# Kernel optimization log

Hardware: AMD Instinct MI355X
Metric: run time of the kernel (lower is better)

Reference implementation:

```python
import jax, jax.numpy as jnp
import numpy as np

N = 8192
NHID = 256

def setup_inputs() -> dict:
    key = jax.random.key(0)
    ks = jax.random.split(key, 9)
    s = 1.0 / np.sqrt(NHID)  # torch Linear default init scale
    return {
        "x1": jax.random.normal(ks[0], (N, NHID), jnp.float32),
        "x2": jax.random.normal(ks[1], (N, NHID), jnp.float32),
        "x3": jax.random.normal(ks[2], (N, NHID), jnp.float32),
        "Wq": jax.random.uniform(ks[3], (NHID, NHID), jnp.float32, -s, s),
        "bq": jax.random.uniform(ks[4], (NHID,), jnp.float32, -s, s),
        "Wk": jax.random.uniform(ks[5], (NHID, NHID), jnp.float32, -s, s),
        "bk": jax.random.uniform(ks[6], (NHID,), jnp.float32, -s, s),
        "Wv": jax.random.uniform(ks[7], (NHID, NHID), jnp.float32, -s, s),
        "bv": jax.random.uniform(ks[8], (NHID,), jnp.float32, -s, s),
    }

def reference(x1, x2, x3, Wq, bq, Wk, bk, Wv, bv):
    # torch.nn.Linear: y = x @ W.T + b
    q = x1 @ Wq.T + bq                      # [N, nhid]
    k = x2 @ Wk.T + bk                      # [N, nhid]
    v = x3 @ Wv.T + bv                      # [N, nhid]
    scores = q @ k.T                        # [N, N], NOTE: unscaled (no 1/sqrt(d))
    attn = jax.nn.softmax(scores, axis=1)   # softmax over keys (dim=1)
    return attn @ v                         # [N, nhid]
```

## Files before the change

### kernel.cpp

```cpp
#include <hip/hip_runtime.h>
#include <stdint.h>

typedef unsigned short u16;
typedef __attribute__((ext_vector_type(8))) short short8;
typedef __attribute__((ext_vector_type(4))) float f32x4;

#define LOG2E 1.4426950408889634f
#define NT 8192
#define DH 256

#define QH     0
#define KH     2097152
#define VTB    4194304
#define OPARTB 6291456
#define XH0 6291456
#define XL0 8388608
#define XH1 10485760
#define XL1 12582912
#define XH2 14680064
#define XL2 16777216
#define WQH 18874368
#define WQL 18939904
#define WKH 19005440
#define WKL 19070976
#define WVH 19136512
#define WVL 19202048
#define MPART_F 11534336
#define LPART_F 11599872

__device__ __forceinline__ u16 f2bf(float f) {
  union { float f; uint32_t u; } c; c.f = f;
  uint32_t u = c.u;
  return (u16)((u + 0x7fffu + ((u >> 16) & 1)) >> 16);
}
__device__ __forceinline__ u16 f2bf_hu(float f) {
  union { float f; uint32_t u; } c; c.f = f;
  return (u16)((c.u + 0x8000u) >> 16);
}
__device__ __forceinline__ float bf2f(u16 h) {
  union { uint32_t u; float f; } c; c.u = ((uint32_t)h) << 16;
  return c.f;
}

__device__ __forceinline__ int swz32(int u, int row) {
  return (u & 24) | ((u & 7) ^ (row & 7));
}

__device__ __forceinline__ f32x4 mfma16(short8 a, short8 b, f32x4 c) {
  return __builtin_amdgcn_mfma_f32_16x16x32_bf16(a, b, c, 0, 0, 0);
}

__device__ __forceinline__ void gl_lds16(const u16* g, u16* l) {
  __builtin_amdgcn_global_load_lds(
      (const __attribute__((address_space(1))) uint32_t*)g,
      (__attribute__((address_space(3))) uint32_t*)l, 16, 0, 0);
}

__global__ __launch_bounds__(256) void k_convert(
    const float* __restrict__ x1, const float* __restrict__ x2, const float* __restrict__ x3,
    const float* __restrict__ wq, const float* __restrict__ wk, const float* __restrict__ wv,
    u16* __restrict__ wsu) {
  int b = blockIdx.x;
  const float* src; u16 *dh, *dl; int bl;
  if (b < 1024)      { src = x1; dh = wsu + XH0; dl = wsu + XL0; bl = b; }
  else if (b < 2048) { src = x2; dh = wsu + XH1; dl = wsu + XL1; bl = b - 1024; }
  else if (b < 3072) { src = x3; dh = wsu + XH2; dl = wsu + XL2; bl = b - 2048; }
  else if (b < 3104) { src = wq; dh = wsu + WQH; dl = wsu + WQL; bl = b - 3072; }
  else if (b < 3136) { src = wk; dh = wsu + WKH; dl = wsu + WKL; bl = b - 3104; }
  else               { src = wv; dh = wsu + WVH; dl = wsu + WVL; bl = b - 3136; }
  int i = (bl * 256 + threadIdx.x) * 8;
  f32x4 a = *(const f32x4*)(src + i);
  f32x4 c = *(const f32x4*)(src + i + 4);
  short8 rh, rl;
  float v[8] = {a[0], a[1], a[2], a[3], c[0], c[1], c[2], c[3]};
#pragma unroll
  for (int j = 0; j < 8; j++) {
    u16 h = f2bf(v[j]);
    rh[j] = (short)h;
    rl[j] = (short)f2bf(v[j] - bf2f(h));
  }
  *(short8*)(dh + i) = rh;
  *(short8*)(dl + i) = rl;
}

__global__ __launch_bounds__(256) void k_qkv(
    u16* __restrict__ wsu,
    const float* __restrict__ bq, const float* __restrict__ bk, const float* __restrict__ bv) {
  __shared__ u16 sAh[32 * 256];
  __shared__ u16 sAl[32 * 256];
  int bx = blockIdx.x;
  int mid = bx >> 8;
  int t = bx & 255;
  const u16 *Ah, *Al, *Bh, *Bl; u16 *O; const float* bias;
  int rowA0, col0, ldO, biasRow;
  if (mid == 0) {
    Ah = wsu + XH0; Al = wsu + XL0; Bh = wsu + WQH; Bl = wsu + WQL;
    O = wsu + QH; bias = bq; biasRow = 0; ldO = 256;
    rowA0 = t * 32; col0 = 0;
  } else if (mid == 1) {
    Ah = wsu + XH1; Al = wsu + XL1; Bh = wsu + WKH; Bl = wsu + WKL;
    O = wsu + KH; bias = bk; biasRow = 0; ldO = 256;
    rowA0 = t * 32; col0 = 0;
  } else {
    Ah = wsu + WVH; Al = wsu + WVL; Bh = wsu + XH2; Bl = wsu + XL2;
    O = wsu + VTB; bias = bv; biasRow = 1; ldO = 8192;
    rowA0 = (t & 7) * 32; col0 = (t >> 3) * 256;
  }

  int tid = threadIdx.x;
#pragma unroll
  for (int i = 0; i < 4; i++) {
    int L = i * 256 + tid;
    int row = L >> 5, u = L & 31;
    short8 vh = *(const short8*)(Ah + (size_t)(rowA0 + row) * 256 + u * 8);
    short8 vl = *(const short8*)(Al + (size_t)(rowA0 + row) * 256 + u * 8);
    *(short8*)(&sAh[row * 256 + swz32(u, row) * 8]) = vh;
    *(short8*)(&sAl[row * 256 + swz32(u, row) * 8]) = vl;
  }
  __syncthreads();

  int lane = tid & 63, wave = tid >> 6;
  int n = lane & 15, quad = lane >> 4;

#pragma unroll 1
  for (int itc = 0; itc < 4; itc++) {
    int colg = col0 + itc * 64 + wave * 16 + n;
    const u16* pBh = Bh + (size_t)colg * 256 + quad * 8;
    const u16* pBl = Bl + (size_t)colg * 256 + quad * 8;
    f32x4 acc0 = {0.f,0.f,0.f,0.f}, acc1 = {0.f,0.f,0.f,0.f};
#pragma unroll
    for (int kk = 0; kk < 8; kk++) {
      int su = swz32(kk * 4 + quad, n) * 8;
      short8 a0h = *(const short8*)(&sAh[n * 256 + su]);
      short8 a1h = *(const short8*)(&sAh[(n + 16) * 256 + su]);
      short8 a0l = *(const short8*)(&sAl[n * 256 + su]);
      short8 a1l = *(const short8*)(&sAl[(n + 16) * 256 + su]);
      short8 bh  = *(const short8*)(pBh + kk * 32);
      short8 bl  = *(const short8*)(pBl + kk * 32);
      acc0 = mfma16(a0h, bh, acc0);
      acc1 = mfma16(a1h, bh, acc1);
      acc0 = mfma16(a0h, bl, acc0);
      acc1 = mfma16(a1h, bl, acc1);
      acc0 = mfma16(a0l, bh, acc0);
      acc1 = mfma16(a1l, bh, acc1);
    }
    float bcol = biasRow ? 0.0f : bias[colg];
#pragma unroll
    for (int mt = 0; mt < 2; mt++) {
      f32x4 acc = mt ? acc1 : acc0;
#pragma unroll
      for (int r = 0; r < 4; r++) {
        int rowg = rowA0 + mt * 16 + quad * 4 + r;
        float bb = biasRow ? bias[rowg] : bcol;
        O[(size_t)rowg * ldO + colg] = f2bf(acc[r] + bb);
      }
    }
  }
}

__global__ __launch_bounds__(256, 2) void k_flash(
    const u16* __restrict__ wsu, u16* __restrict__ opart, float* __restrict__ wsf) {
  __shared__ u16 sK[2][32 * 256];
  __shared__ u16 sV[2][256 * 32];
  __shared__ u16 sP[4 * 32 * 40];

  int qb = blockIdx.x >> 3, sp = blockIdx.x & 7;
  int tid = threadIdx.x, lane = tid & 63, wave = tid >> 6;
  int n = lane & 15, quad = lane >> 4;
  const u16* Qp = wsu + QH;
  const u16* Kp = wsu + KH;
  const u16* Vp = wsu + VTB;

  short8 qf[2][8];
  int rowQ0 = qb * 128 + wave * 32 + n;
#pragma unroll
  for (int mt = 0; mt < 2; mt++)
#pragma unroll
    for (int kk = 0; kk < 8; kk++)
      qf[mt][kk] = *(const short8*)(Qp + (size_t)(rowQ0 + mt * 16) * 256 + kk * 32 + quad * 8);

  int krow_base = wave * 2 + (lane >> 5);
  int kgu = (lane & 24) | ((lane & 7) ^ (krow_base & 7));
  int vd_base = wave * 16 + (lane >> 2);
  int vgu = (lane & 3) ^ ((lane >> 3) & 3);

  int key00 = sp * 1024;

#pragma unroll
  for (int i = 0; i < 4; i++) {
    gl_lds16(Kp + (size_t)(key00 + i * 8 + krow_base) * 256 + kgu * 8,
             &sK[0][i * 2048 + wave * 512]);
    gl_lds16(Vp + (size_t)(i * 64 + vd_base) * 8192 + key00 + vgu * 8,
             &sV[0][i * 2048 + wave * 512]);
  }

  f32x4 o[2][16];
#pragma unroll
  for (int mt = 0; mt < 2; mt++)
#pragma unroll
    for (int nt = 0; nt < 16; nt++) { o[mt][nt][0]=0.f; o[mt][nt][1]=0.f; o[mt][nt][2]=0.f; o[mt][nt][3]=0.f; }
  float negm0L[8], lcur[8];
#pragma unroll
  for (int j = 0; j < 8; j++) { negm0L[j] = 0.f; lcur[j] = 0.f; }

  for (int it = 0; it < 32; it++) {
    __syncthreads();
    int cur = it & 1;
    if (it + 1 < 32) {
      int k1 = key00 + (it + 1) * 32;
#pragma unroll
      for (int i = 0; i < 4; i++) {
        gl_lds16(Kp + (size_t)(k1 + i * 8 + krow_base) * 256 + kgu * 8,
                 &sK[cur ^ 1][i * 2048 + wave * 512]);
        gl_lds16(Vp + (size_t)(i * 64 + vd_base) * 8192 + k1 + vgu * 8,
                 &sV[cur ^ 1][i * 2048 + wave * 512]);
      }
    }

    f32x4 s00={0.f,0.f,0.f,0.f}, s01={0.f,0.f,0.f,0.f};
    f32x4 s10={0.f,0.f,0.f,0.f}, s11={0.f,0.f,0.f,0.f};
#pragma unroll
    for (int kk = 0; kk < 8; kk++) {
      int su = swz32(kk * 4 + quad, n) * 8;
      short8 b0 = *(const short8*)(&sK[cur][n * 256 + su]);
      short8 b1 = *(const short8*)(&sK[cur][(n + 16) * 256 + su]);
      s00 = mfma16(qf[0][kk], b0, s00);
      s01 = mfma16(qf[0][kk], b1, s01);
      s10 = mfma16(qf[1][kk], b0, s10);
      s11 = mfma16(qf[1][kk], b1, s11);
    }

    if (it == 0) {
#pragma unroll
      for (int mt = 0; mt < 2; mt++)
#pragma unroll
        for (int r = 0; r < 4; r++) {
          float v = mt ? fmaxf(s10[r], s11[r]) : fmaxf(s00[r], s01[r]);
          v = fmaxf(v, __shfl_xor(v, 1));
          v = fmaxf(v, __shfl_xor(v, 2));
          v = fmaxf(v, __shfl_xor(v, 4));
          v = fmaxf(v, __shfl_xor(v, 8));
          negm0L[mt * 4 + r] = -v * LOG2E;
        }
    }

    u16* myP = &sP[wave * 1280];
#pragma unroll
    for (int mt = 0; mt < 2; mt++)
#pragma unroll
      for (int r = 0; r < 4; r++) {
        int j = mt * 4 + r;
        float sv0 = mt ? s10[r] : s00[r];
        float sv1 = mt ? s11[r] : s01[r];
        float x0 = fminf(fmaf(sv0, LOG2E, negm0L[j]), 110.f);
        float x1 = fminf(fmaf(sv1, LOG2E, negm0L[j]), 110.f);
        float p0 = exp2f(x0);
        float p1 = exp2f(x1);
        lcur[j] += p0 + p1;
        int row = mt * 16 + quad * 4 + r;
        myP[row * 40 + n] = f2bf_hu(p0);
        myP[row * 40 + 16 + n] = f2bf_hu(p1);
      }

    u16* myP2 = &sP[wave * 1280];
    short8 pa0 = *(const short8*)(&myP2[n * 40 + quad * 8]);
    short8 pa1 = *(const short8*)(&myP2[(16 + n) * 40 + quad * 8]);
#pragma unroll
    for (int nt = 0; nt < 16; nt++) {
      int d = nt * 16 + n;
      short8 vb = *(const short8*)(&sV[cur][d * 32 + (quad ^ ((n >> 1) & 3)) * 8]);
      o[0][nt] = mfma16(pa0, vb, o[0][nt]);
      o[1][nt] = mfma16(pa1, vb, o[1][nt]);
    }
  }

#pragma unroll
  for (int j = 0; j < 8; j++) {
    float v = lcur[j];
    v += __shfl_xor(v, 1); v += __shfl_xor(v, 2);
    v += __shfl_xor(v, 4); v += __shfl_xor(v, 8);
    lcur[j] = v;
  }

  u16* op = opart + (size_t)sp * (NT * DH);
  int rowb = qb * 128 + wave * 32;
#pragma unroll
  for (int mt = 0; mt < 2; mt++)
#pragma unroll
    for (int nt = 0; nt < 16; nt++)
#pragma unroll
      for (int r = 0; r < 4; r++) {
        int row = rowb + mt * 16 + quad * 4 + r;
        op[(size_t)row * 256 + nt * 16 + n] = f2bf(o[mt][nt][r]);
      }
  if (n == 0) {
#pragma unroll
    for (int j = 0; j < 8; j++) {
      int row = rowb + (j >> 2) * 16 + quad * 4 + (j & 3);
      wsf[MPART_F + sp * NT + row] = negm0L[j] * -0.6931471805599453f;
      wsf[LPART_F + sp * NT + row] = lcur[j];
    }
  }
}

__global__ __launch_bounds__(256) void k_combine(
    const u16* __restrict__ opart, const float* __restrict__ wsf, float* __restrict__ out) {
  int gid = blockIdx.x * 256 + threadIdx.x;
  int row = gid >> 6, cg = gid & 63;
  float m[8], l[8];
#pragma unroll
  for (int s = 0; s < 8; s++) {
    m[s] = wsf[MPART_F + s * NT + row];
    l[s] = wsf[LPART_F + s * NT + row];
  }
  float ms = m[0];
#pragma unroll
  for (int s = 1; s < 8; s++) ms = fmaxf(ms, m[s]);
  float denom = 0.f;
  float acc[4] = {0.f, 0.f, 0.f, 0.f};
#pragma unroll
  for (int s = 0; s < 8; s++) {
    float w = exp2f((m[s] - ms) * LOG2E);
    denom += w * l[s];
    const u16* pp = opart + ((size_t)s * NT + row) * 256 + cg * 4;
    uint2 v = *(const uint2*)pp;
    acc[0] += w * bf2f((u16)(v.x & 0xffff));
    acc[1] += w * bf2f((u16)(v.x >> 16));
    acc[2] += w * bf2f((u16)(v.y & 0xffff));
    acc[3] += w * bf2f((u16)(v.y >> 16));
  }
  float inv = 1.0f / denom;
  f32x4 r = {acc[0] * inv, acc[1] * inv, acc[2] * inv, acc[3] * inv};
  *(f32x4*)(out + (size_t)row * 256 + cg * 4) = r;
}

extern "C" void kernel_launch(void* const* d_in, const int* in_sizes, int n_in,
                              void* d_out, int out_size, void* d_ws, size_t ws_size,
                              hipStream_t stream) {
  const float* x1 = (const float*)d_in[0];
  const float* x2 = (const float*)d_in[1];
  const float* x3 = (const float*)d_in[2];
  const float* Wq = (const float*)d_in[3];
  const float* bq = (const float*)d_in[4];
  const float* Wk = (const float*)d_in[5];
  const float* bk = (const float*)d_in[6];
  const float* Wv = (const float*)d_in[7];
  const float* bv = (const float*)d_in[8];
  u16* wsu = (u16*)d_ws;
  float* wsf = (float*)d_ws;
  float* out = (float*)d_out;

  k_convert<<<dim3(3168), dim3(256), 0, stream>>>(x1, x2, x3, Wq, Wk, Wv, wsu);
  k_qkv<<<dim3(768), dim3(256), 0, stream>>>(wsu, bq, bk, bv);
  k_flash<<<dim3(512), dim3(256), 0, stream>>>(wsu, wsu + OPARTB, wsf);
  k_combine<<<dim3(2048), dim3(256), 0, stream>>>(wsu + OPARTB, wsf, out);
}
```

Before: 223.8 us.

## Load K and V fragments directly from global memory instead of LDS staging

```diff
diff --git a/kernel.cpp b/kernel.cpp
--- a/kernel.cpp
+++ b/kernel.cpp
@@ -48,12 +48,6 @@
 
 __device__ __forceinline__ f32x4 mfma16(short8 a, short8 b, f32x4 c) {
   return __builtin_amdgcn_mfma_f32_16x16x32_bf16(a, b, c, 0, 0, 0);
-}
-
-__device__ __forceinline__ void gl_lds16(const u16* g, u16* l) {
-  __builtin_amdgcn_global_load_lds(
-      (const __attribute__((address_space(1))) uint32_t*)g,
-      (__attribute__((address_space(3))) uint32_t*)l, 16, 0, 0);
 }
 
 __global__ __launch_bounds__(256) void k_convert(
@@ -160,8 +154,6 @@
 
 __global__ __launch_bounds__(256, 2) void k_flash(
     const u16* __restrict__ wsu, u16* __restrict__ opart, float* __restrict__ wsf) {
-  __shared__ u16 sK[2][32 * 256];
-  __shared__ u16 sV[2][256 * 32];
   __shared__ u16 sP[4 * 32 * 40];
 
   int qb = blockIdx.x >> 3, sp = blockIdx.x & 7;
@@ -179,21 +171,6 @@
     for (int kk = 0; kk < 8; kk++)
       qf[mt][kk] = *(const short8*)(Qp + (size_t)(rowQ0 + mt * 16) * 256 + kk * 32 + quad * 8);
 
-  int krow_base = wave * 2 + (lane >> 5);
-  int kgu = (lane & 24) | ((lane & 7) ^ (krow_base & 7));
-  int vd_base = wave * 16 + (lane >> 2);
-  int vgu = (lane & 3) ^ ((lane >> 3) & 3);
-
-  int key00 = sp * 1024;
-
-#pragma unroll
-  for (int i = 0; i < 4; i++) {
-    gl_lds16(Kp + (size_t)(key00 + i * 8 + krow_base) * 256 + kgu * 8,
-             &sK[0][i * 2048 + wave * 512]);
-    gl_lds16(Vp + (size_t)(i * 64 + vd_base) * 8192 + key00 + vgu * 8,
-             &sV[0][i * 2048 + wave * 512]);
-  }
-
   f32x4 o[2][16];
 #pragma unroll
   for (int mt = 0; mt < 2; mt++)
@@ -203,27 +180,21 @@
 #pragma unroll
   for (int j = 0; j < 8; j++) { negm0L[j] = 0.f; lcur[j] = 0.f; }
 
+  int koff = n * 512 + quad * 8;
+  int voff = n * 8192 + quad * 8;
+  u16* myP = &sP[wave * 1280];
+
   for (int it = 0; it < 32; it++) {
-    __syncthreads();
-    int cur = it & 1;
-    if (it + 1 < 32) {
-      int k1 = key00 + (it + 1) * 32;
-#pragma unroll
-      for (int i = 0; i < 4; i++) {
-        gl_lds16(Kp + (size_t)(k1 + i * 8 + krow_base) * 256 + kgu * 8,
-                 &sK[cur ^ 1][i * 2048 + wave * 512]);
-        gl_lds16(Vp + (size_t)(i * 64 + vd_base) * 8192 + k1 + vgu * 8,
-                 &sV[cur ^ 1][i * 2048 + wave * 512]);
-      }
-    }
+    int key0 = sp * 1024 + it * 32;
+    const u16* kb = Kp + (size_t)key0 * 256;
+    const u16* vb = Vp + key0;
 
     f32x4 s00={0.f,0.f,0.f,0.f}, s01={0.f,0.f,0.f,0.f};
     f32x4 s10={0.f,0.f,0.f,0.f}, s11={0.f,0.f,0.f,0.f};
 #pragma unroll
     for (int kk = 0; kk < 8; kk++) {
-      int su = swz32(kk * 4 + quad, n) * 8;
-      short8 b0 = *(const short8*)(&sK[cur][n * 256 + su]);
-      short8 b1 = *(const short8*)(&sK[cur][(n + 16) * 256 + su]);
+      short8 b0 = *(const short8*)(kb + koff + kk * 32);
+      short8 b1 = *(const short8*)(kb + koff + 256 + kk * 32);
       s00 = mfma16(qf[0][kk], b0, s00);
       s01 = mfma16(qf[0][kk], b1, s01);
       s10 = mfma16(qf[1][kk], b0, s10);
@@ -244,7 +215,6 @@
         }
     }
 
-    u16* myP = &sP[wave * 1280];
 #pragma unroll
     for (int mt = 0; mt < 2; mt++)
 #pragma unroll
@@ -252,25 +222,21 @@
         int j = mt * 4 + r;
         float sv0 = mt ? s10[r] : s00[r];
         float sv1 = mt ? s11[r] : s01[r];
-        float x0 = fminf(fmaf(sv0, LOG2E, negm0L[j]), 110.f);
-        float x1 = fminf(fmaf(sv1, LOG2E, negm0L[j]), 110.f);
-        float p0 = exp2f(x0);
-        float p1 = exp2f(x1);
+        float p0 = exp2f(fmaf(sv0, LOG2E, negm0L[j]));
+        float p1 = exp2f(fmaf(sv1, LOG2E, negm0L[j]));
         lcur[j] += p0 + p1;
         int row = mt * 16 + quad * 4 + r;
-        myP[row * 40 + n] = f2bf_hu(p0);
-        myP[row * 40 + 16 + n] = f2bf_hu(p1);
+        uint32_t pk = (uint32_t)f2bf_hu(p0) | ((uint32_t)f2bf_hu(p1) << 16);
+        *(uint32_t*)&myP[row * 40 + 2 * n] = pk;
       }
 
-    u16* myP2 = &sP[wave * 1280];
-    short8 pa0 = *(const short8*)(&myP2[n * 40 + quad * 8]);
-    short8 pa1 = *(const short8*)(&myP2[(16 + n) * 40 + quad * 8]);
+    short8 pa0 = *(const short8*)(&myP[n * 40 + quad * 8]);
+    short8 pa1 = *(const short8*)(&myP[(16 + n) * 40 + quad * 8]);
 #pragma unroll
     for (int nt = 0; nt < 16; nt++) {
-      int d = nt * 16 + n;
-      short8 vb = *(const short8*)(&sV[cur][d * 32 + (quad ^ ((n >> 1) & 3)) * 8]);
-      o[0][nt] = mfma16(pa0, vb, o[0][nt]);
-      o[1][nt] = mfma16(pa1, vb, o[1][nt]);
+      short8 vbf = *(const short8*)(vb + (size_t)nt * 131072 + voff);
+      o[0][nt] = mfma16(pa0, vbf, o[0][nt]);
+      o[1][nt] = mfma16(pa1, vbf, o[1][nt]);
     }
   }
 
```

Result: slower. 382.9 us (+71.1%).

## Stage QKV weight tiles in LDS and interleave K rows for packed P stores

Applied to the files above, without the earlier changes.

```diff
diff --git a/kernel.cpp b/kernel.cpp
--- a/kernel.cpp
+++ b/kernel.cpp
@@ -42,8 +42,8 @@
   return c.f;
 }
 
-__device__ __forceinline__ int swz32(int u, int row) {
-  return (u & 24) | ((u & 7) ^ (row & 7));
+__device__ __forceinline__ int swz32(int u, int h) {
+  return (u & 24) | ((u & 7) ^ (h & 7));
 }
 
 __device__ __forceinline__ f32x4 mfma16(short8 a, short8 b, f32x4 c) {
@@ -88,26 +88,32 @@
     const float* __restrict__ bq, const float* __restrict__ bk, const float* __restrict__ bv) {
   __shared__ u16 sAh[32 * 256];
   __shared__ u16 sAl[32 * 256];
+  __shared__ u16 sBh[32 * 256];
+  __shared__ u16 sBl[32 * 256];
   int bx = blockIdx.x;
   int mid = bx >> 8;
   int t = bx & 255;
   const u16 *Ah, *Al, *Bh, *Bl; u16 *O; const float* bias;
-  int rowA0, col0, ldO, biasRow;
+  int rowA0, colBase, ldO, biasRow;
   if (mid == 0) {
     Ah = wsu + XH0; Al = wsu + XL0; Bh = wsu + WQH; Bl = wsu + WQL;
     O = wsu + QH; bias = bq; biasRow = 0; ldO = 256;
-    rowA0 = t * 32; col0 = 0;
+    rowA0 = t * 32; colBase = 0;
   } else if (mid == 1) {
     Ah = wsu + XH1; Al = wsu + XL1; Bh = wsu + WKH; Bl = wsu + WKL;
     O = wsu + KH; bias = bk; biasRow = 0; ldO = 256;
-    rowA0 = t * 32; col0 = 0;
+    rowA0 = t * 32; colBase = 0;
   } else {
     Ah = wsu + WVH; Al = wsu + WVL; Bh = wsu + XH2; Bl = wsu + XL2;
     O = wsu + VTB; bias = bv; biasRow = 1; ldO = 8192;
-    rowA0 = (t & 7) * 32; col0 = (t >> 3) * 256;
+    rowA0 = (t & 7) * 32; colBase = (t >> 3) * 256;
   }
 
   int tid = threadIdx.x;
+  int lane = tid & 63, wave = tid >> 6;
+  int n = lane & 15, quad = lane >> 4;
+  int wm = wave >> 1, wn = wave & 1;
+
 #pragma unroll
   for (int i = 0; i < 4; i++) {
     int L = i * 256 + tid;
@@ -117,43 +123,51 @@
     *(short8*)(&sAh[row * 256 + swz32(u, row) * 8]) = vh;
     *(short8*)(&sAl[row * 256 + swz32(u, row) * 8]) = vl;
   }
-  __syncthreads();
-
-  int lane = tid & 63, wave = tid >> 6;
-  int n = lane & 15, quad = lane >> 4;
+
+  int brow0 = wave * 2 + (lane >> 5);
+  int bgu = (lane & 24) | ((lane & 7) ^ (brow0 & 7));
+
+#pragma unroll
+  for (int i = 0; i < 4; i++) {
+    gl_lds16(Bh + (size_t)(colBase + i * 8 + brow0) * 256 + bgu * 8, &sBh[i * 2048 + wave * 512]);
+    gl_lds16(Bl + (size_t)(colBase + i * 8 + brow0) * 256 + bgu * 8, &sBl[i * 2048 + wave * 512]);
+  }
 
 #pragma unroll 1
-  for (int itc = 0; itc < 4; itc++) {
-    int colg = col0 + itc * 64 + wave * 16 + n;
-    const u16* pBh = Bh + (size_t)colg * 256 + quad * 8;
-    const u16* pBl = Bl + (size_t)colg * 256 + quad * 8;
-    f32x4 acc0 = {0.f,0.f,0.f,0.f}, acc1 = {0.f,0.f,0.f,0.f};
+  for (int g = 0; g < 8; g++) {
+    __syncthreads();
+
+    int colg = colBase + g * 32 + wn * 16 + n;
+    f32x4 acc = {0.f, 0.f, 0.f, 0.f};
 #pragma unroll
     for (int kk = 0; kk < 8; kk++) {
-      int su = swz32(kk * 4 + quad, n) * 8;
-      short8 a0h = *(const short8*)(&sAh[n * 256 + su]);
-      short8 a1h = *(const short8*)(&sAh[(n + 16) * 256 + su]);
-      short8 a0l = *(const short8*)(&sAl[n * 256 + su]);
-      short8 a1l = *(const short8*)(&sAl[(n + 16) * 256 + su]);
-      short8 bh  = *(const short8*)(pBh + kk * 32);
-      short8 bl  = *(const short8*)(pBl + kk * 32);
-      acc0 = mfma16(a0h, bh, acc0);
-      acc1 = mfma16(a1h, bh, acc1);
-      acc0 = mfma16(a0h, bl, acc0);
-      acc1 = mfma16(a1h, bl, acc1);
-      acc0 = mfma16(a0l, bh, acc0);
-      acc1 = mfma16(a1l, bh, acc1);
-    }
+      int ra = wm * 16 + n;
+      int rbB = wn * 16 + n;
+      short8 ah = *(const short8*)(&sAh[ra * 256 + swz32(kk * 4 + quad, ra) * 8]);
+      short8 al = *(const short8*)(&sAl[ra * 256 + swz32(kk * 4 + quad, ra) * 8]);
+      short8 bh = *(const short8*)(&sBh[rbB * 256 + swz32(kk * 4 + quad, rbB) * 8]);
+      short8 bl = *(const short8*)(&sBl[rbB * 256 + swz32(kk * 4 + quad, rbB) * 8]);
+      acc = mfma16(ah, bh, acc);
+      acc = mfma16(ah, bl, acc);
+      acc = mfma16(al, bh, acc);
+    }
+
+    if (g < 7) {
+      __syncthreads();
+      int b0 = colBase + (g + 1) * 32;
+#pragma unroll
+      for (int i = 0; i < 4; i++) {
+        gl_lds16(Bh + (size_t)(b0 + i * 8 + brow0) * 256 + bgu * 8, &sBh[i * 2048 + wave * 512]);
+        gl_lds16(Bl + (size_t)(b0 + i * 8 + brow0) * 256 + bgu * 8, &sBl[i * 2048 + wave * 512]);
+      }
+    }
+
     float bcol = biasRow ? 0.0f : bias[colg];
 #pragma unroll
-    for (int mt = 0; mt < 2; mt++) {
-      f32x4 acc = mt ? acc1 : acc0;
-#pragma unroll
-      for (int r = 0; r < 4; r++) {
-        int rowg = rowA0 + mt * 16 + quad * 4 + r;
-        float bb = biasRow ? bias[rowg] : bcol;
-        O[(size_t)rowg * ldO + colg] = f2bf(acc[r] + bb);
-      }
+    for (int r = 0; r < 4; r++) {
+      int rowg = rowA0 + wm * 16 + quad * 4 + r;
+      float bb = biasRow ? bias[rowg] : bcol;
+      O[(size_t)rowg * ldO + colg] = f2bf(acc[r] + bb);
     }
   }
 }
@@ -179,8 +193,10 @@
     for (int kk = 0; kk < 8; kk++)
       qf[mt][kk] = *(const short8*)(Qp + (size_t)(rowQ0 + mt * 16) * 256 + kk * 32 + quad * 8);
 
-  int krow_base = wave * 2 + (lane >> 5);
-  int kgu = (lane & 24) | ((lane & 7) ^ (krow_base & 7));
+  int krow0 = wave * 2 + (lane >> 5);
+  int kh0 = (krow0 >> 1) & 7;
+  int kgu0 = (lane & 24) | ((lane & 7) ^ kh0);
+  int kgu1 = kgu0 ^ 4;
   int vd_base = wave * 16 + (lane >> 2);
   int vgu = (lane & 3) ^ ((lane >> 3) & 3);
 
@@ -188,7 +204,8 @@
 
 #pragma unroll
   for (int i = 0; i < 4; i++) {
-    gl_lds16(Kp + (size_t)(key00 + i * 8 + krow_base) * 256 + kgu * 8,
+    int ku = (i & 1) ? kgu1 : kgu0;
+    gl_lds16(Kp + (size_t)(key00 + i * 8 + krow0) * 256 + ku * 8,
              &sK[0][i * 2048 + wave * 512]);
     gl_lds16(Vp + (size_t)(i * 64 + vd_base) * 8192 + key00 + vgu * 8,
              &sV[0][i * 2048 + wave * 512]);
@@ -210,7 +227,8 @@
       int k1 = key00 + (it + 1) * 32;
 #pragma unroll
       for (int i = 0; i < 4; i++) {
-        gl_lds16(Kp + (size_t)(k1 + i * 8 + krow_base) * 256 + kgu * 8,
+        int ku = (i & 1) ? kgu1 : kgu0;
+        gl_lds16(Kp + (size_t)(k1 + i * 8 + krow0) * 256 + ku * 8,
                  &sK[cur ^ 1][i * 2048 + wave * 512]);
         gl_lds16(Vp + (size_t)(i * 64 + vd_base) * 8192 + k1 + vgu * 8,
                  &sV[cur ^ 1][i * 2048 + wave * 512]);
@@ -222,8 +240,8 @@
 #pragma unroll
     for (int kk = 0; kk < 8; kk++) {
       int su = swz32(kk * 4 + quad, n) * 8;
-      short8 b0 = *(const short8*)(&sK[cur][n * 256 + su]);
-      short8 b1 = *(const short8*)(&sK[cur][(n + 16) * 256 + su]);
+      short8 b0 = *(const short8*)(&sK[cur][(2 * n) * 256 + su]);
+      short8 b1 = *(const short8*)(&sK[cur][(2 * n) * 256 + 256 + su]);
       s00 = mfma16(qf[0][kk], b0, s00);
       s01 = mfma16(qf[0][kk], b1, s01);
       s10 = mfma16(qf[1][kk], b0, s10);
@@ -258,13 +276,12 @@
         float p1 = exp2f(x1);
         lcur[j] += p0 + p1;
         int row = mt * 16 + quad * 4 + r;
-        myP[row * 40 + n] = f2bf_hu(p0);
-        myP[row * 40 + 16 + n] = f2bf_hu(p1);
+        uint32_t pk = (uint32_t)f2bf_hu(p0) | ((uint32_t)f2bf_hu(p1) << 16);
+        *(uint32_t*)&myP[row * 40 + 2 * n] = pk;
       }
 
-    u16* myP2 = &sP[wave * 1280];
-    short8 pa0 = *(const short8*)(&myP2[n * 40 + quad * 8]);
-    short8 pa1 = *(const short8*)(&myP2[(16 + n) * 40 + quad * 8]);
+    short8 pa0 = *(const short8*)(&myP[n * 40 + quad * 8]);
+    short8 pa1 = *(const short8*)(&myP[(16 + n) * 40 + quad * 8]);
 #pragma unroll
     for (int nt = 0; nt < 16; nt++) {
       int d = nt * 16 + n;
```

New measurement: 217.6 us. 2.8% less time.
